# Kernel optimization log

Measured on AMD Instinct MI355X. Metric: run time of the kernel, lower is better.

Reference implementation:

```python
import jax, jax.numpy as jnp
import numpy as np
import math

EMB = 64
NEG_INF = -1e30

def _layernorm(x, g, b, eps=1e-5):
    mu = jnp.mean(x, axis=-1, keepdims=True)
    var = jnp.mean((x - mu) ** 2, axis=-1, keepdims=True)
    return (x - mu) * jax.lax.rsqrt(var + eps) * g + b

def setup_inputs() -> dict:
    key = jax.random.key(0)
    ks = jax.random.split(key, 8)
    b, t, n, d = 16, 12, 307, EMB
    s = 1.0 / math.sqrt(d)
    inp = {
        'x': jax.random.normal(ks[0], (b, t, n, d), dtype=jnp.float32),
        'stg': jax.random.uniform(ks[1], (b, n, t, n), dtype=jnp.float32),
        'topk': 3,
        'q_w': jax.random.normal(ks[2], (d, d), dtype=jnp.float32) * s,
        'q_b': jnp.zeros((d,), jnp.float32),
        'k_w': jax.random.normal(ks[3], (d, d), dtype=jnp.float32) * s,
        'k_b': jnp.zeros((d,), jnp.float32),
        'ln_g': jnp.ones((d,), jnp.float32),
        'ln_b': jnp.zeros((d,), jnp.float32),
        'ffn_ln_g': jnp.ones((d,), jnp.float32),
        'ffn_ln_b': jnp.zeros((d,), jnp.float32),
        'fc1_w': jax.random.normal(ks[4], (4 * d, d), dtype=jnp.float32) * s,
        'fc1_b': jnp.zeros((4 * d,), jnp.float32),
        'fc2_w': jax.random.normal(ks[5], (d, 4 * d), dtype=jnp.float32) * (0.5 * s),
        'fc2_b': jnp.zeros((d,), jnp.float32),
    }
    return inp

def reference(x, stg, topk, q_w, q_b, k_w, k_b, ln_g, ln_b, ffn_ln_g, ffn_ln_b, fc1_w, fc1_b, fc2_w, fc2_b):
    b, t, n, d = x.shape
    scale = 1.0 / math.sqrt(d)
    x_ = _layernorm(x, ln_g, ln_b)           # [b,t,n,d]
    y_ = x_[:, -1]                            # [b,n,d] last timestep
    q = y_ @ q_w.T + q_b                      # [b,n,d]
    k = x_ @ k_w.T + k_b                      # [b,t,n,d]
    dg = jnp.einsum('bnd,btmd->bntm', q, k) * scale
    sag = jax.nn.sigmoid(dg) * stg * scale    # gated scores [b,n,t,n]
    sag = sag.reshape(b, n, t * n)
    if topk > 0:
        kk = topk * n if topk < 5 else topk   # mirrors torch's self.topk *= n
        top_values, _ = jax.lax.top_k(sag, kk)
        thr = top_values[..., -1:]
        sag = jnp.where(sag > thr, sag, NEG_INF)  # strict >, as in torch code
    sag = jax.nn.softmax(sag, axis=-1).reshape(b, n, t, n)  # dropout in eval mode = identity
    o = jnp.einsum('bntm,btmd->bnd', sag, x_)
    h = o + y_
    # FFN: pre-norm residual MLP (LayerNorm -> Linear(d,4d) -> ReLU -> Linear(4d,d) + residual)
    z = _layernorm(h, ffn_ln_g, ffn_ln_b)
    z = jax.nn.relu(z @ fc1_w.T + fc1_b) @ fc2_w.T + fc2_b
    return h + z
```

## Files before the change

### kernel.cpp

```cpp
#include <hip/hip_runtime.h>

typedef __bf16 bf16x8 __attribute__((ext_vector_type(8)));
typedef float  f32x4  __attribute__((ext_vector_type(4)));
typedef unsigned short u16x8 __attribute__((ext_vector_type(8)));
typedef unsigned short u16x4 __attribute__((ext_vector_type(4)));

constexpr int BB    = 16;
constexpr int TT    = 12;
constexpr int NN    = 307;
constexpr int TN    = TT * NN;
constexpr int ROWSX = BB * TT * NN;
constexpr int ROWSH = BB * NN;
constexpr int SST1  = 3712;
constexpr int SSTR  = 3840;
constexpr int HPS   = ROWSH * 64;
constexpr int KQ    = 928;
constexpr int WBS   = 152;
constexpr float SCALE = 0.125f;

__device__ __forceinline__ float wred_sum(float v) {
#pragma unroll
    for (int m = 32; m > 0; m >>= 1) v += __shfl_xor(v, m, 64);
    return v;
}

__global__ void fold_k(const float* __restrict__ qw, const float* __restrict__ qb,
                       const float* __restrict__ kw, const float* __restrict__ kb,
                       float* __restrict__ M, float* __restrict__ b2,
                       float* __restrict__ vv, float* __restrict__ cc) {
    int e = blockIdx.x, d = threadIdx.x;
    float acc = 0.f;
    for (int dp = 0; dp < 64; ++dp) acc += qw[dp * 64 + e] * kw[dp * 64 + d];
    M[e * 64 + d] = acc;
    float vp = wred_sum(qw[d * 64 + e] * kb[d]);
    if (d == 0) vv[e] = vp;
    if (e == 0) {
        float b = 0.f;
        for (int dp = 0; dp < 64; ++dp) b += qb[dp] * kw[dp * 64 + d];
        b2[d] = b;
        float cp = wred_sum(qb[d] * kb[d]);
        if (d == 0) *cc = cp;
    }
}

__global__ void wconv_k(const float* __restrict__ fc1w, const float* __restrict__ fc2w,
                        __bf16* __restrict__ fc1b16, __bf16* __restrict__ fc2b16) {
    int i = blockIdx.x * 256 + threadIdx.x;
    if (i < 16384) fc1b16[i] = (__bf16)fc1w[i];
    else fc2b16[i - 16384] = (__bf16)fc2w[i - 16384];
}

__global__ __launch_bounds__(256) void ln_k(const float* __restrict__ x,
                                            const float* __restrict__ g,
                                            const float* __restrict__ b,
                                            __bf16* __restrict__ xnb,
                                            float* __restrict__ y32) {
    int w = threadIdx.x >> 6, l = threadIdx.x & 63;
    int r = blockIdx.x * 4 + w;
    if (r >= ROWSX) return;
    float val = x[r * 64 + l];
    float mu  = wred_sum(val) * (1.f / 64.f);
    float dv  = val - mu;
    float var = wred_sum(dv * dv) * (1.f / 64.f);
    float xv  = dv * rsqrtf(var + 1e-5f) * g[l] + b[l];
    xnb[(size_t)r * 64 + l] = (__bf16)xv;
    int t = (r / NN) % TT;
    if (t == TT - 1) {
        int bbv = r / (NN * TT), n = r % NN;
        y32[(bbv * NN + n) * 64 + l] = xv;
    }
}

__global__ __launch_bounds__(256) void t_k(const __bf16* __restrict__ xnb,
                                           __bf16* __restrict__ xnT) {
    __shared__ unsigned short tile[64][65];
    int bb = blockIdx.y, j0 = blockIdx.x * 64, t = threadIdx.x;
    const unsigned short* src = (const unsigned short*)xnb;
    unsigned short* dst = (unsigned short*)xnT;
#pragma unroll
    for (int i = 0; i < 16; ++i) {
        int f = t + 256 * i, jr = f >> 6, dc = f & 63;
        int j = j0 + jr;
        tile[jr][dc] = (j < TN) ? src[((size_t)bb * TN + j) * 64 + dc] : (unsigned short)0;
    }
    __syncthreads();
#pragma unroll
    for (int i = 0; i < 16; ++i) {
        int f = t + 256 * i, d = f >> 6, jj = f & 63;
        dst[((size_t)bb * 64 + d) * SSTR + j0 + jj] = tile[jj][d];
    }
}

__global__ __launch_bounds__(256) void qt_k(const float* __restrict__ y32,
                                            const float* __restrict__ M,
                                            const float* __restrict__ b2,
                                            const float* __restrict__ vv,
                                            const float* __restrict__ ccp,
                                            __bf16* __restrict__ qtb,
                                            float* __restrict__ cq) {
    int w = threadIdx.x >> 6, l = threadIdx.x & 63;
    int rr = blockIdx.x * 4 + w;
    if (rr >= ROWSH) return;
    float y = y32[rr * 64 + l];
    float acc = b2[l];
#pragma unroll
    for (int e = 0; e < 64; ++e) acc += __shfl(y, e, 64) * M[e * 64 + l];
    qtb[(size_t)rr * 64 + l] = (__bf16)acc;
    float cp = wred_sum(y * vv[l]);
    if (l == 0) cq[rr] = cp + *ccp;
}

__global__ __launch_bounds__(256, 4) void score_k(const __bf16* __restrict__ qtb,
                                                  const float* __restrict__ cq,
                                                  const __bf16* __restrict__ xnb,
                                                  const float* __restrict__ stg,
                                                  __bf16* __restrict__ sag) {
    __shared__ unsigned short wb[64 * WBS];
    int bb = blockIdx.z, n0 = blockIdx.y * 64, j0 = blockIdx.x * 128;
    int t = threadIdx.x;
    int w = t >> 6, lane = t & 63;
    int m16 = lane & 15, q4 = lane >> 4;

    const float* stgb = stg + (size_t)bb * NN * TN;
    float4 sv[4][2];
    float cn[4];
#pragma unroll
    for (int nt = 0; nt < 4; ++nt) {
        int n = n0 + nt * 16 + m16;
        const float* srow = stgb + (size_t)min(n, NN - 1) * TN;
#pragma unroll
        for (int jj = 0; jj < 2; ++jj) {
            int jb = j0 + (w * 2 + jj) * 16 + q4 * 4;
            float4 s4 = {0.f, 0.f, 0.f, 0.f};
            if (jb < TN) s4 = *(const float4*)(srow + jb);
            sv[nt][jj] = s4;
        }
        int nc = n0 + nt * 16 + m16;
        cn[nt] = 0.f;
    }
#pragma unroll
    for (int nt = 0; nt < 4; ++nt) {
        int n = n0 + nt * 16 + m16;
        cn[nt] = (n < NN) ? cq[bb * NN + n] : 0.f;
    }

    bf16x8 a[2][2];
#pragma unroll
    for (int jj = 0; jj < 2; ++jj) {
        const bf16x8* ap = (const bf16x8*)(xnb + ((size_t)bb * TN + j0 + (w * 2 + jj) * 16 + m16) * 64);
        a[jj][0] = ap[q4];
        a[jj][1] = ap[q4 + 4];
    }

    f32x4 acc[2][4];
#pragma unroll
    for (int nt = 0; nt < 4; ++nt) {
        const bf16x8* bp = (const bf16x8*)(qtb + ((size_t)bb * NN + n0 + nt * 16 + m16) * 64);
        bf16x8 b0 = bp[q4], b1 = bp[q4 + 4];
#pragma unroll
        for (int jj = 0; jj < 2; ++jj) {
            f32x4 c = {0.f, 0.f, 0.f, 0.f};
            c = __builtin_amdgcn_mfma_f32_16x16x32_bf16(a[jj][0], b0, c, 0, 0, 0);
            c = __builtin_amdgcn_mfma_f32_16x16x32_bf16(a[jj][1], b1, c, 0, 0, 0);
            acc[jj][nt] = c;
        }
    }

#pragma unroll
    for (int nt = 0; nt < 4; ++nt) {
#pragma unroll
        for (int jj = 0; jj < 2; ++jj) {
            int jb = j0 + (w * 2 + jj) * 16 + q4 * 4;
            float svv[4] = {sv[nt][jj].x, sv[nt][jj].y, sv[nt][jj].z, sv[nt][jj].w};
            u16x4 hw;
#pragma unroll
            for (int r = 0; r < 4; ++r) {
                float dg = (acc[jj][nt][r] + cn[nt]) * SCALE;
                float s  = 1.f / (1.f + __expf(-dg));
                float wv = (jb + r < TN) ? s * svv[r] * SCALE : 0.f;
                __bf16 wb16 = (__bf16)wv;
                hw[r] = *(unsigned short*)&wb16;
            }
            *(u16x4*)&wb[(nt * 16 + m16) * WBS + (w * 2 + jj) * 16 + q4 * 4] = hw;
        }
    }
    __syncthreads();

#pragma unroll
    for (int i = 0; i < 4; ++i) {
        int chunk = t + i * 256;
        int row = chunk >> 4, c8 = (chunk & 15) * 8;
        int n = n0 + row;
        if (n < NN) {
            u16x8 v = *(const u16x8*)&wb[row * WBS + c8];
            *(u16x8*)((unsigned short*)sag + (size_t)(bb * NN + n) * SST1 + j0 + c8) = v;
        }
    }
}

__global__ __launch_bounds__(256) void smax_k(__bf16* __restrict__ sagB,
                                              const int* __restrict__ topk_p,
                                              float* __restrict__ rsum) {
    int t = threadIdx.x;
    int wid = t >> 6, lane = t & 63;
    int row = blockIdx.x * 4 + wid;
    if (row >= ROWSH) return;

    int topkv = *topk_p;
    bool selAll = (topkv <= 0);
    int kk = 0;
    if (!selAll) {
        kk = (topkv < 5) ? topkv * NN : topkv;
        if (kk > TN) kk = TN;
    }

    u16x8* src = (u16x8*)((unsigned short*)sagB + (size_t)row * SST1);
    u16x8 va[8];
#pragma unroll
    for (int ci = 0; ci < 8; ++ci) {
        int c = lane + (ci << 6);
        u16x8 v = {0, 0, 0, 0, 0, 0, 0, 0};
        if (c < 464) v = src[c];
        va[ci] = v;
    }
    int vmb = 0;
#pragma unroll
    for (int ci = 0; ci < 8; ++ci)
#pragma unroll
        for (int e = 0; e < 8; ++e) vmb = max(vmb, (int)va[ci][e]);
#pragma unroll
    for (int m = 32; m > 0; m >>= 1) vmb = max(vmb, __shfl_xor(vmb, m, 64));
    float vmax = __uint_as_float(((unsigned)vmb) << 16);

    unsigned thrb = 0;
    if (!selAll) {
        unsigned lo = 0, hi = (unsigned)vmb;
        while (lo < hi) {
            unsigned mid = (lo + hi) >> 1;
            int cnt = 0;
#pragma unroll
            for (int ci = 0; ci < 8; ++ci)
#pragma unroll
                for (int e = 0; e < 8; ++e)
                    cnt += (int)__popcll(__ballot((unsigned)va[ci][e] > mid));
            if (cnt < kk) hi = mid; else lo = mid + 1;
        }
        thrb = lo;
    }

    float local = 0.f;
#pragma unroll
    for (int ci = 0; ci < 8; ++ci) {
        int c = lane + (ci << 6);
        int nvv = (c < 460) ? 8 : ((c == 460) ? 4 : 0);
#pragma unroll
        for (int e = 0; e < 8; ++e) {
            unsigned u = va[ci][e];
            bool sel = selAll ? (e < nvv) : (u > thrb);
            float ev = sel ? __expf(__uint_as_float(u << 16) - vmax) : 0.f;
            local += ev;
            __bf16 eb = (__bf16)ev;
            va[ci][e] = *(unsigned short*)&eb;
        }
    }
    local = wred_sum(local);
    bool uni = !(local > 0.f);
    if (lane == 0) rsum[row] = uni ? (float)TN : local;

    if (uni) {
        __bf16 one = (__bf16)1.f, zero = (__bf16)0.f;
#pragma unroll
        for (int ci = 0; ci < 8; ++ci) {
            int c = lane + (ci << 6);
            if (c < 464) {
                int nvv = (c < 460) ? 8 : ((c == 460) ? 4 : 0);
                bf16x8 o;
#pragma unroll
                for (int e = 0; e < 8; ++e) o[e] = (e < nvv) ? one : zero;
                *(bf16x8*)&src[c] = o;
            }
        }
    } else {
#pragma unroll
        for (int ci = 0; ci < 8; ++ci) {
            int c = lane + (ci << 6);
            if (c < 464) src[c] = va[ci];
        }
    }
}

__global__ __launch_bounds__(256) void pv_k(const __bf16* __restrict__ sagB,
                                            const __bf16* __restrict__ xnT,
                                            const float* __restrict__ y32,
                                            const float* __restrict__ rsum,
                                            float* __restrict__ hp) {
    int bb = blockIdx.z, kq = blockIdx.y, n0 = blockIdx.x * 16;
    int wid = threadIdx.x >> 6, lane = threadIdx.x & 63;
    int m16 = lane & 15, q4 = lane >> 4;

    int arow = min(n0 + m16, NN - 1);
    const __bf16* ab  = sagB + (size_t)(bb * NN + arow) * SST1 + kq * KQ + q4 * 8;
    const __bf16* bbp = xnT + ((size_t)bb * 64 + wid * 16 + m16) * SSTR + kq * KQ + q4 * 8;

    f32x4 acc0 = {0.f, 0.f, 0.f, 0.f}, acc1 = {0.f, 0.f, 0.f, 0.f};
#pragma unroll 4
    for (int ks = 0; ks < 29; ++ks) {
        bf16x8 a = *(const bf16x8*)(ab + ks * 32);
        bf16x8 b = *(const bf16x8*)(bbp + ks * 32);
        if (ks & 1) acc1 = __builtin_amdgcn_mfma_f32_16x16x32_bf16(a, b, acc1, 0, 0, 0);
        else        acc0 = __builtin_amdgcn_mfma_f32_16x16x32_bf16(a, b, acc0, 0, 0, 0);
    }
#pragma unroll
    for (int r = 0; r < 4; ++r) {
        int n = n0 + q4 * 4 + r;
        if (n < NN) {
            size_t o = (size_t)(bb * NN + n) * 64 + wid * 16 + m16;
            float inv = 1.f / rsum[bb * NN + n];
            float v = (acc0[r] + acc1[r]) * inv;
            if (kq == 0) v += y32[o];
            hp[(size_t)kq * HPS + o] = v;
        }
    }
}

__global__ __launch_bounds__(256) void ffn_k(const float* __restrict__ hp,
                                             const float* __restrict__ g,
                                             const float* __restrict__ bln,
                                             const __bf16* __restrict__ fc1b16,
                                             const float* __restrict__ fc1b,
                                             const __bf16* __restrict__ fc2b16,
                                             const float* __restrict__ fc2b,
                                             float* __restrict__ out) {
    __shared__ __bf16 zb[16 * 68];
    __shared__ __bf16 ab[16 * 264];
    int t = threadIdx.x, r0 = blockIdx.x * 16;
    int wid = t >> 6, lane = t & 63;
    int m16 = lane & 15, q4 = lane >> 4;

#pragma unroll
    for (int q = 0; q < 4; ++q) {
        int rl = wid * 4 + q;
        size_t i = (size_t)(r0 + rl) * 64 + lane;
        float val = hp[i] + hp[HPS + i] + hp[2 * HPS + i] + hp[3 * HPS + i];
        float mu  = wred_sum(val) * (1.f / 64.f);
        float dv  = val - mu;
        float var = wred_sum(dv * dv) * (1.f / 64.f);
        zb[rl * 68 + lane] = (__bf16)(dv * rsqrtf(var + 1e-5f) * g[lane] + bln[lane]);
    }
    __syncthreads();

    bf16x8 a0 = *(const bf16x8*)&zb[m16 * 68 + q4 * 8];
    bf16x8 a1 = *(const bf16x8*)&zb[m16 * 68 + 32 + q4 * 8];
#pragma unroll
    for (int jt2 = 0; jt2 < 4; ++jt2) {
        int j0t = (wid * 4 + jt2) * 16;
        const __bf16* bp = fc1b16 + (size_t)(j0t + m16) * 64 + q4 * 8;
        f32x4 c = {0.f, 0.f, 0.f, 0.f};
        c = __builtin_amdgcn_mfma_f32_16x16x32_bf16(a0, *(const bf16x8*)bp, c, 0, 0, 0);
        c = __builtin_amdgcn_mfma_f32_16x16x32_bf16(a1, *(const bf16x8*)(bp + 32), c, 0, 0, 0);
        int j = j0t + m16;
        float bias = fc1b[j];
#pragma unroll
        for (int r = 0; r < 4; ++r)
            ab[(q4 * 4 + r) * 264 + j] = (__bf16)fmaxf(c[r] + bias, 0.f);
    }
    __syncthreads();

    f32x4 c2a = {0.f, 0.f, 0.f, 0.f}, c2b = {0.f, 0.f, 0.f, 0.f};
    const __bf16* b2p = fc2b16 + (size_t)(wid * 16 + m16) * 256 + q4 * 8;
#pragma unroll
    for (int k8 = 0; k8 < 8; k8 += 2) {
        bf16x8 aa0 = *(const bf16x8*)&ab[m16 * 264 + k8 * 32 + q4 * 8];
        bf16x8 aa1 = *(const bf16x8*)&ab[m16 * 264 + (k8 + 1) * 32 + q4 * 8];
        c2a = __builtin_amdgcn_mfma_f32_16x16x32_bf16(aa0, *(const bf16x8*)(b2p + k8 * 32), c2a, 0, 0, 0);
        c2b = __builtin_amdgcn_mfma_f32_16x16x32_bf16(aa1, *(const bf16x8*)(b2p + (k8 + 1) * 32), c2b, 0, 0, 0);
    }
    int d = wid * 16 + m16;
    float bias2 = fc2b[d];
#pragma unroll
    for (int r = 0; r < 4; ++r) {
        size_t row = (size_t)(r0 + q4 * 4 + r);
        size_t o = row * 64 + d;
        float hsum = hp[o] + hp[HPS + o] + hp[2 * HPS + o] + hp[3 * HPS + o];
        out[o] = hsum + c2a[r] + c2b[r] + bias2;
    }
}

extern "C" void kernel_launch(void* const* d_in, const int* in_sizes, int n_in,
                              void* d_out, int out_size, void* d_ws, size_t ws_size,
                              hipStream_t stream) {
    const float* x    = (const float*)d_in[0];
    const float* stg  = (const float*)d_in[1];
    const int*   topk = (const int*)d_in[2];
    const float* qw   = (const float*)d_in[3];
    const float* qb   = (const float*)d_in[4];
    const float* kw   = (const float*)d_in[5];
    const float* kb   = (const float*)d_in[6];
    const float* lng  = (const float*)d_in[7];
    const float* lnb  = (const float*)d_in[8];
    const float* flng = (const float*)d_in[9];
    const float* flnb = (const float*)d_in[10];
    const float* fc1w = (const float*)d_in[11];
    const float* fc1b = (const float*)d_in[12];
    const float* fc2w = (const float*)d_in[13];
    const float* fc2b = (const float*)d_in[14];
    float* out = (float*)d_out;

    float* ws = (float*)d_ws;
    __bf16* xnb = (__bf16*)ws;
    float* p1   = ws + 1886208;
    __bf16* xnT = (__bf16*)p1;
    float* p2   = p1 + 1966080;
    __bf16* qtb = (__bf16*)p2;
    float* y32  = p2 + 157696;
    float* cq   = y32 + 314368;
    float* M    = cq + 4928;
    float* b2   = M + 4096;
    float* vv   = b2 + 64;
    float* cc   = vv + 64;
    __bf16* fc1b16 = (__bf16*)(cc + 16);
    __bf16* fc2b16 = (__bf16*)((float*)fc1b16 + 8192);
    __bf16* sag = (__bf16*)((float*)fc2b16 + 8192);
    float* hp   = (float*)sag + 9116672;
    float* rsum = hp + 4 * HPS;

    fold_k<<<64, 64, 0, stream>>>(qw, qb, kw, kb, M, b2, vv, cc);
    wconv_k<<<128, 256, 0, stream>>>(fc1w, fc2w, fc1b16, fc2b16);
    ln_k<<<(ROWSX + 3) / 4, 256, 0, stream>>>(x, lng, lnb, xnb, y32);
    t_k<<<dim3((TN + 63) / 64, BB), 256, 0, stream>>>(xnb, xnT);
    qt_k<<<(ROWSH + 3) / 4, 256, 0, stream>>>(y32, M, b2, vv, cc, qtb, cq);
    score_k<<<dim3((TN + 127) / 128, (NN + 63) / 64, BB), 256, 0, stream>>>(qtb, cq, xnb, stg, sag);
    smax_k<<<(ROWSH + 3) / 4, 256, 0, stream>>>(sag, topk, rsum);
    pv_k<<<dim3((NN + 15) / 16, 4, BB), 256, 0, stream>>>(sag, xnT, y32, rsum, hp);
    ffn_k<<<ROWSH / 16, 256, 0, stream>>>(hp, flng, flnb, fc1b16, fc1b, fc2b16, fc2b, out);
}
```

Before: 256.5 us.

## Recompute softmax exponentials inside PV kernel instead of rewriting score buffer

The softmax kernel no longer writes exponentiated bf16 probabilities back to the score buffer. It stores only per-row max, threshold and sum, and the PV matmul recomputes the masked exponentials on the fly from raw scores. This removes a full write pass over the large score matrix (about 36 MB of bf16). In exchange, each PV block redoes the exp work, and since four warps share each A row the exponentials are recomputed several times. A uniform-row case is encoded as a negative sum.

```diff
diff --git a/kernel.cpp b/kernel.cpp
--- a/kernel.cpp
+++ b/kernel.cpp
@@ -135,12 +135,6 @@
             if (jb < TN) s4 = *(const float4*)(srow + jb);
             sv[nt][jj] = s4;
         }
-        int nc = n0 + nt * 16 + m16;
-        cn[nt] = 0.f;
-    }
-#pragma unroll
-    for (int nt = 0; nt < 4; ++nt) {
-        int n = n0 + nt * 16 + m16;
         cn[nt] = (n < NN) ? cq[bb * NN + n] : 0.f;
     }
 
@@ -198,9 +192,11 @@
     }
 }
 
-__global__ __launch_bounds__(256) void smax_k(__bf16* __restrict__ sagB,
+__global__ __launch_bounds__(256) void smax_k(const __bf16* __restrict__ sagB,
                                               const int* __restrict__ topk_p,
-                                              float* __restrict__ rsum) {
+                                              float* __restrict__ rsum,
+                                              float* __restrict__ vmaxf,
+                                              unsigned* __restrict__ thrv) {
     int t = threadIdx.x;
     int wid = t >> 6, lane = t & 63;
     int row = blockIdx.x * 4 + wid;
@@ -214,7 +210,7 @@
         if (kk > TN) kk = TN;
     }
 
-    u16x8* src = (u16x8*)((unsigned short*)sagB + (size_t)row * SST1);
+    const u16x8* src = (const u16x8*)((const unsigned short*)sagB + (size_t)row * SST1);
     u16x8 va[8];
 #pragma unroll
     for (int ci = 0; ci < 8; ++ci) {
@@ -257,35 +253,15 @@
         for (int e = 0; e < 8; ++e) {
             unsigned u = va[ci][e];
             bool sel = selAll ? (e < nvv) : (u > thrb);
-            float ev = sel ? __expf(__uint_as_float(u << 16) - vmax) : 0.f;
-            local += ev;
-            __bf16 eb = (__bf16)ev;
-            va[ci][e] = *(unsigned short*)&eb;
+            local += sel ? __expf(__uint_as_float(u << 16) - vmax) : 0.f;
         }
     }
     local = wred_sum(local);
-    bool uni = !(local > 0.f);
-    if (lane == 0) rsum[row] = uni ? (float)TN : local;
-
-    if (uni) {
-        __bf16 one = (__bf16)1.f, zero = (__bf16)0.f;
-#pragma unroll
-        for (int ci = 0; ci < 8; ++ci) {
-            int c = lane + (ci << 6);
-            if (c < 464) {
-                int nvv = (c < 460) ? 8 : ((c == 460) ? 4 : 0);
-                bf16x8 o;
-#pragma unroll
-                for (int e = 0; e < 8; ++e) o[e] = (e < nvv) ? one : zero;
-                *(bf16x8*)&src[c] = o;
-            }
-        }
-    } else {
-#pragma unroll
-        for (int ci = 0; ci < 8; ++ci) {
-            int c = lane + (ci << 6);
-            if (c < 464) src[c] = va[ci];
-        }
+    if (lane == 0) {
+        bool uni = !(local > 0.f);
+        rsum[row]  = uni ? -(float)TN : local;
+        vmaxf[row] = vmax;
+        thrv[row]  = thrb;
     }
 }
 
@@ -293,29 +269,50 @@
                                             const __bf16* __restrict__ xnT,
                                             const float* __restrict__ y32,
                                             const float* __restrict__ rsum,
+                                            const float* __restrict__ vmaxf,
+                                            const unsigned* __restrict__ thrv,
+                                            const int* __restrict__ topk_p,
                                             float* __restrict__ hp) {
     int bb = blockIdx.z, kq = blockIdx.y, n0 = blockIdx.x * 16;
     int wid = threadIdx.x >> 6, lane = threadIdx.x & 63;
     int m16 = lane & 15, q4 = lane >> 4;
 
+    bool selAll = (*topk_p <= 0);
     int arow = min(n0 + m16, NN - 1);
-    const __bf16* ab  = sagB + (size_t)(bb * NN + arow) * SST1 + kq * KQ + q4 * 8;
+    int ridx = bb * NN + arow;
+    float rsA   = rsum[ridx];
+    bool  uniA  = rsA < 0.f;
+    float vmaxA = vmaxf[ridx];
+    unsigned thrA = thrv[ridx];
+
+    const __bf16* ab  = sagB + (size_t)ridx * SST1 + kq * KQ + q4 * 8;
     const __bf16* bbp = xnT + ((size_t)bb * 64 + wid * 16 + m16) * SSTR + kq * KQ + q4 * 8;
 
     f32x4 acc0 = {0.f, 0.f, 0.f, 0.f}, acc1 = {0.f, 0.f, 0.f, 0.f};
 #pragma unroll 4
     for (int ks = 0; ks < 29; ++ks) {
-        bf16x8 a = *(const bf16x8*)(ab + ks * 32);
+        u16x8 ub = *(const u16x8*)(ab + ks * 32);
         bf16x8 b = *(const bf16x8*)(bbp + ks * 32);
-        if (ks & 1) acc1 = __builtin_amdgcn_mfma_f32_16x16x32_bf16(a, b, acc1, 0, 0, 0);
-        else        acc0 = __builtin_amdgcn_mfma_f32_16x16x32_bf16(a, b, acc0, 0, 0, 0);
+        int jb = kq * KQ + ks * 32 + q4 * 8;
+        bf16x8 aw;
+#pragma unroll
+        for (int e = 0; e < 8; ++e) {
+            unsigned u = ub[e];
+            bool valid = (jb + e) < TN;
+            bool sel = selAll ? valid : (u > thrA);
+            float ev = sel ? __expf(__uint_as_float(u << 16) - vmaxA) : 0.f;
+            ev = uniA ? (valid ? 1.f : 0.f) : ev;
+            aw[e] = (__bf16)ev;
+        }
+        if (ks & 1) acc1 = __builtin_amdgcn_mfma_f32_16x16x32_bf16(aw, b, acc1, 0, 0, 0);
+        else        acc0 = __builtin_amdgcn_mfma_f32_16x16x32_bf16(aw, b, acc0, 0, 0, 0);
     }
 #pragma unroll
     for (int r = 0; r < 4; ++r) {
         int n = n0 + q4 * 4 + r;
         if (n < NN) {
             size_t o = (size_t)(bb * NN + n) * 64 + wid * 16 + m16;
-            float inv = 1.f / rsum[bb * NN + n];
+            float inv = 1.f / fabsf(rsum[bb * NN + n]);
             float v = (acc0[r] + acc1[r]) * inv;
             if (kq == 0) v += y32[o];
             hp[(size_t)kq * HPS + o] = v;
@@ -423,6 +420,8 @@
     __bf16* sag = (__bf16*)((float*)fc2b16 + 8192);
     float* hp   = (float*)sag + 9116672;
     float* rsum = hp + 4 * HPS;
+    float* vmaxf = rsum + 4928;
+    unsigned* thrv = (unsigned*)(vmaxf + 4928);
 
     fold_k<<<64, 64, 0, stream>>>(qw, qb, kw, kb, M, b2, vv, cc);
     wconv_k<<<128, 256, 0, stream>>>(fc1w, fc2w, fc1b16, fc2b16);
@@ -430,7 +429,7 @@
     t_k<<<dim3((TN + 63) / 64, BB), 256, 0, stream>>>(xnb, xnT);
     qt_k<<<(ROWSH + 3) / 4, 256, 0, stream>>>(y32, M, b2, vv, cc, qtb, cq);
     score_k<<<dim3((TN + 127) / 128, (NN + 63) / 64, BB), 256, 0, stream>>>(qtb, cq, xnb, stg, sag);
-    smax_k<<<(ROWSH + 3) / 4, 256, 0, stream>>>(sag, topk, rsum);
-    pv_k<<<dim3((NN + 15) / 16, 4, BB), 256, 0, stream>>>(sag, xnT, y32, rsum, hp);
+    smax_k<<<(ROWSH + 3) / 4, 256, 0, stream>>>(sag, topk, rsum, vmaxf, thrv);
+    pv_k<<<dim3((NN + 15) / 16, 4, BB), 256, 0, stream>>>(sag, xnT, y32, rsum, vmaxf, thrv, topk, hp);
     ffn_k<<<ROWSH / 16, 256, 0, stream>>>(hp, flng, flnb, fc1b16, fc1b, fc2b16, fc2b, out);
 }
```

Result: no change. 261.0 us (+1.7%).
